# Kernel optimization log

Hardware: AMD Instinct MI355X
Metric: run time of the kernel (lower is better)

Reference implementation:

```python
import jax, jax.numpy as jnp
import numpy as np

B, S, I, H, C = 256, 128, 512, 1024, 10
VOCAB = S  # nn.Embedding(seq_length, input_dim)


def _lstm_dir(embeds_tbi, W, b):
    """Run an LSTM over time. embeds_tbi: [S,B,I]; W: [4H, I+H] stacked (g,i,f,o); b: [4H]."""
    h0 = jnp.zeros((B, H), jnp.float32)
    c0 = jnp.zeros((B, H), jnp.float32)

    def step(carry, x_t):
        c, h = carry
        xh = jnp.concatenate([x_t, h], axis=1)          # [B, I+H]
        z = xh @ W.T + b                                 # [B, 4H]
        g, i, f, o = jnp.split(z, 4, axis=1)
        g = jnp.tanh(g)
        i = jax.nn.sigmoid(i)
        f = jax.nn.sigmoid(f)
        o = jax.nn.sigmoid(o)
        new_c = g * i + c * f
        new_h = jnp.tanh(new_c) * o
        return (new_c, new_h), None

    (c_T, h_T), _ = jax.lax.scan(step, (c0, h0), embeds_tbi)
    return h_T


def setup_inputs() -> dict:
    key = jax.random.key(0)
    ks = jax.random.split(key, 8)
    x = jax.random.randint(ks[0], (B, S), 0, VOCAB)
    embed = jax.random.normal(ks[1], (VOCAB, I), jnp.float32) * 0.5
    scale = 1.0 / np.sqrt(I + H)
    fwd_W = jax.random.normal(ks[2], (4 * H, I + H), jnp.float32) * scale  # stacked g,i,f,o
    fwd_b = jax.random.normal(ks[3], (4 * H,), jnp.float32) * 0.02
    bwd_W = jax.random.normal(ks[4], (4 * H, I + H), jnp.float32) * scale
    bwd_b = jax.random.normal(ks[5], (4 * H,), jnp.float32) * 0.02
    p_w = jax.random.normal(ks[6], (C, 2 * H), jnp.float32) * (1.0 / np.sqrt(2 * H))
    p_b = jax.random.normal(ks[7], (C,), jnp.float32) * 0.02
    return {"x": x, "embed": embed, "fwd_W": fwd_W, "fwd_b": fwd_b,
            "bwd_W": bwd_W, "bwd_b": bwd_b, "p_w": p_w, "p_b": p_b}


def reference(x, embed, fwd_W, fwd_b, bwd_W, bwd_b, p_w, p_b):
    embeds = embed[x]                       # [B,S,I]
    emb_t = jnp.transpose(embeds, (1, 0, 2))  # [S,B,I]
    h_fwd = _lstm_dir(emb_t, fwd_W, fwd_b)
    h_bwd = _lstm_dir(emb_t[::-1], bwd_W, bwd_b)
    h_comb = jnp.concatenate([h_fwd, h_bwd], axis=1)  # [B,2H]
    return jax.nn.log_softmax(h_comb @ p_w.T + p_b, axis=1)
```

## Files before the change

kernel.cpp:

```cpp
#include <hip/hip_runtime.h>
#include <hip/hip_bf16.h>
#include <math.h>

#define B 256
#define S 128
#define I_DIM 512
#define H 1024
#define C 10
#define WROW 1536

#define LDS_H 131072

typedef float f32x4 __attribute__((ext_vector_type(4), may_alias));
typedef __bf16 bf16x8 __attribute__((ext_vector_type(8), may_alias));
typedef unsigned int u32x4 __attribute__((ext_vector_type(4), may_alias));
typedef unsigned long long u64;

__device__ __forceinline__ unsigned short f2bf(float f) {
    union { float f; unsigned u; } a; a.f = f;
    return (unsigned short)((a.u + 0x7fffu + ((a.u >> 16) & 1u)) >> 16);
}
__device__ __forceinline__ float sigf(float v) { return 1.0f / (1.0f + __expf(-v)); }
__device__ __forceinline__ float tanh_fast(float v) { return 1.0f - 2.0f / (1.0f + __expf(2.0f * v)); }

__global__ void wf_build(const float* __restrict__ fwd_W,
                         const float* __restrict__ bwd_W,
                         __hip_bfloat16* __restrict__ wF) {
    int gid = blockIdx.x * 256 + threadIdx.x;
    int lane = gid & 63, kk = (gid >> 6) & 31, nsub = (gid >> 11) & 255, d = gid >> 19;
    int n_gl = nsub * 16 + (lane & 15);
    int j = n_gl >> 2, g = n_gl & 3;
    int k = kk * 32 + (lane >> 4) * 8;
    const float* W = d ? bwd_W : fwd_W;
    const float* src = W + (size_t)(g * 1024 + j) * WROW + I_DIM + k;
    ushort4 lo = make_ushort4(f2bf(src[0]), f2bf(src[1]), f2bf(src[2]), f2bf(src[3]));
    ushort4 hi = make_ushort4(f2bf(src[4]), f2bf(src[5]), f2bf(src[6]), f2bf(src[7]));
    ushort4* dst = (ushort4*)(wF + (size_t)gid * 8);
    dst[0] = lo; dst[1] = hi;
}

__global__ void projp_kernel(const float* __restrict__ embed,
                             const float* __restrict__ fwd_W,
                             const float* __restrict__ fwd_b,
                             const float* __restrict__ bwd_W,
                             const float* __restrict__ bwd_b,
                             float* __restrict__ projP) {
    __shared__ float wrows[16][516];
    int d  = blockIdx.x >> 8;
    int nc = blockIdx.x & 255;
    int n0 = nc * 16;
    const float* W    = d ? bwd_W : fwd_W;
    const float* bias = d ? bwd_b : fwd_b;
    int tid = threadIdx.x;
    for (int i = tid; i < 16 * 128; i += 256) {
        int r = i >> 7, kc = i & 127;
        *(f32x4*)&wrows[r][kc * 4] = *(const f32x4*)(W + (size_t)(n0 + r) * WROW + kc * 4);
    }
    __syncthreads();
    const int r = tid & 15, vg = tid >> 4;
    const float* eb = embed + (size_t)(vg * 8) * I_DIM;
    f32x4 acc[8] = {};
    for (int kc = 0; kc < 128; kc++) {
        f32x4 w = *(const f32x4*)&wrows[r][kc * 4];
#pragma unroll
        for (int vi = 0; vi < 8; vi++) {
            f32x4 e = *(const f32x4*)(eb + (size_t)vi * I_DIM + kc * 4);
            acc[vi] += w * e;
        }
    }
    const int n = n0 + r, g = n >> 10, j = n & 1023;
    const float bv = bias[n];
    float* outp = projP + ((size_t)d * 1024 + j) * 128 * 4 + g;
#pragma unroll
    for (int vi = 0; vi < 8; vi++) {
        float s = acc[vi][0] + acc[vi][1] + acc[vi][2] + acc[vi][3] + bv;
        outp[(vg * 8 + vi) * 4] = s;
    }
}

__device__ __forceinline__ void stage8(const __hip_bfloat16* hr, int r0, int cc,
                                       char* smem, int ibase) {
    const void* p0 = (const void*)(hr + (size_t)((ibase + 0) * 4 + r0) * H + cc * 8);
    const void* p1 = (const void*)(hr + (size_t)((ibase + 1) * 4 + r0) * H + cc * 8);
    const void* p2 = (const void*)(hr + (size_t)((ibase + 2) * 4 + r0) * H + cc * 8);
    const void* p3 = (const void*)(hr + (size_t)((ibase + 3) * 4 + r0) * H + cc * 8);
    const void* p4 = (const void*)(hr + (size_t)((ibase + 4) * 4 + r0) * H + cc * 8);
    const void* p5 = (const void*)(hr + (size_t)((ibase + 5) * 4 + r0) * H + cc * 8);
    const void* p6 = (const void*)(hr + (size_t)((ibase + 6) * 4 + r0) * H + cc * 8);
    const void* p7 = (const void*)(hr + (size_t)((ibase + 7) * 4 + r0) * H + cc * 8);
    u32x4 s0, s1, s2, s3, s4, s5, s6, s7;
    asm volatile(
        "global_load_dwordx4 %0, %8, off sc0 sc1\n\t"
        "global_load_dwordx4 %1, %9, off sc0 sc1\n\t"
        "global_load_dwordx4 %2, %10, off sc0 sc1\n\t"
        "global_load_dwordx4 %3, %11, off sc0 sc1\n\t"
        "global_load_dwordx4 %4, %12, off sc0 sc1\n\t"
        "global_load_dwordx4 %5, %13, off sc0 sc1\n\t"
        "global_load_dwordx4 %6, %14, off sc0 sc1\n\t"
        "global_load_dwordx4 %7, %15, off sc0 sc1\n\t"
        "s_waitcnt vmcnt(0)"
        : "=&v"(s0), "=&v"(s1), "=&v"(s2), "=&v"(s3),
          "=&v"(s4), "=&v"(s5), "=&v"(s6), "=&v"(s7)
        : "v"(p0), "v"(p1), "v"(p2), "v"(p3), "v"(p4), "v"(p5), "v"(p6), "v"(p7)
        : "memory");
    int row;
    row = (ibase + 0) * 4 + r0; *(u32x4*)(smem + row * 2048 + ((cc * 16) ^ ((row & 7) << 4))) = s0;
    row = (ibase + 1) * 4 + r0; *(u32x4*)(smem + row * 2048 + ((cc * 16) ^ ((row & 7) << 4))) = s1;
    row = (ibase + 2) * 4 + r0; *(u32x4*)(smem + row * 2048 + ((cc * 16) ^ ((row & 7) << 4))) = s2;
    row = (ibase + 3) * 4 + r0; *(u32x4*)(smem + row * 2048 + ((cc * 16) ^ ((row & 7) << 4))) = s3;
    row = (ibase + 4) * 4 + r0; *(u32x4*)(smem + row * 2048 + ((cc * 16) ^ ((row & 7) << 4))) = s4;
    row = (ibase + 5) * 4 + r0; *(u32x4*)(smem + row * 2048 + ((cc * 16) ^ ((row & 7) << 4))) = s5;
    row = (ibase + 6) * 4 + r0; *(u32x4*)(smem + row * 2048 + ((cc * 16) ^ ((row & 7) << 4))) = s6;
    row = (ibase + 7) * 4 + r0; *(u32x4*)(smem + row * 2048 + ((cc * 16) ^ ((row & 7) << 4))) = s7;
}

__global__ __launch_bounds__(512, 2) void bilstm_persistent(
        const int* __restrict__ x,
        const __hip_bfloat16* __restrict__ wF,
        const float* __restrict__ projP,
        __hip_bfloat16* __restrict__ hbuf,
        unsigned* __restrict__ flags) {
    extern __shared__ char smem[];
    const int bid = blockIdx.x;
    const int xcd = bid & 7;
    const int d = xcd >> 2, jtHi = xcd & 3;
    const int idx = bid >> 3;
    const int jtLo = idx >> 2, bt = idx & 3;
    const int jt = jtHi * 8 + jtLo;
    const int tid = threadIdx.x, wid = tid >> 6, lane = tid & 63;
    const int l15 = lane & 15, l4 = lane >> 4;
    const int b0 = bt * 64;
    const size_t dBH = (size_t)d * B * H;

    const __hip_bfloat16* wp = wF + (size_t)(d * 256 + jt * 8 + wid) * 16384;
    const int j = jt * 32 + wid * 4 + l4;
    const f32x4* pp = (const f32x4*)projP + ((size_t)d * 1024 + j) * 128;
    const int r0 = tid >> 7;
    const int cc = tid & 127;

    int brow[4], bswz[4];
#pragma unroll
    for (int bs = 0; bs < 4; bs++) {
        int row = bs * 16 + l15;
        brow[bs] = row * 2048;
        bswz[bs] = (row & 7) << 4;
    }

    float cst[4] = {0.f, 0.f, 0.f, 0.f};

    for (int t = 0; t < S; t++) {
        if (t > 0) {
            if (tid == 0) {
                const unsigned* p = flags + (size_t)((t - 1) * 8 + d * 4 + bt) * 16;
                while (__hip_atomic_load(p, __ATOMIC_RELAXED, __HIP_MEMORY_SCOPE_AGENT) < 32u)
                    __builtin_amdgcn_s_sleep(4);
            }
            __syncthreads();
        }

        bf16x8 Ap[8];
        if (t > 0) {
#pragma unroll
            for (int p = 0; p < 8; p++)
                Ap[p] = *(const bf16x8*)(wp + p * 512 + lane * 8);
        }
        const int tt = d ? (S - 1 - t) : t;
        int vv[4];
#pragma unroll
        for (int bs = 0; bs < 4; bs++)
            vv[bs] = x[(b0 + bs * 16 + l15) * S + tt];

        if (t > 0) {
            const __hip_bfloat16* hr = hbuf + (size_t)(t & 1) * 2 * B * H + dBH + (size_t)b0 * H;
            stage8(hr, r0, cc, smem, 0);
            stage8(hr, r0, cc, smem, 8);
        }

        f32x4 pj[4];
#pragma unroll
        for (int bs = 0; bs < 4; bs++) pj[bs] = pp[vv[bs]];

        f32x4 acc[4] = {};
        if (t > 0) {
            __syncthreads();
            bf16x8 Bcur[4];
#pragma unroll
            for (int bs = 0; bs < 4; bs++)
                Bcur[bs] = *(const bf16x8*)(smem + brow[bs] + ((l4 * 16) ^ bswz[bs]));
#pragma unroll
            for (int kk = 0; kk < 32; kk++) {
                bf16x8 A = Ap[kk & 7];
                if (kk < 24)
                    Ap[kk & 7] = *(const bf16x8*)(wp + (kk + 8) * 512 + lane * 8);
                bf16x8 B0 = Bcur[0], B1 = Bcur[1], B2 = Bcur[2], B3 = Bcur[3];
                if (kk < 31) {
                    int koff = (kk + 1) * 64 + l4 * 16;
#pragma unroll
                    for (int bs = 0; bs < 4; bs++)
                        Bcur[bs] = *(const bf16x8*)(smem + brow[bs] + (koff ^ bswz[bs]));
                }
                acc[0] = __builtin_amdgcn_mfma_f32_16x16x32_bf16(A, B0, acc[0], 0, 0, 0);
                acc[1] = __builtin_amdgcn_mfma_f32_16x16x32_bf16(A, B1, acc[1], 0, 0, 0);
                acc[2] = __builtin_amdgcn_mfma_f32_16x16x32_bf16(A, B2, acc[2], 0, 0, 0);
                acc[3] = __builtin_amdgcn_mfma_f32_16x16x32_bf16(A, B3, acc[3], 0, 0, 0);
            }
        }

        float hnv[4];
#pragma unroll
        for (int bs = 0; bs < 4; bs++) {
            float zg = acc[bs][0] + pj[bs][0];
            float zi = acc[bs][1] + pj[bs][1];
            float zf = acc[bs][2] + pj[bs][2];
            float zo = acc[bs][3] + pj[bs][3];
            float gg = tanh_fast(zg);
            float ii = sigf(zi);
            float ff = sigf(zf);
            float oo = sigf(zo);
            float cn = gg * ii + cst[bs] * ff;
            cst[bs] = cn;
            hnv[bs] = tanh_fast(cn) * oo;
        }

        unsigned plo = (unsigned)f2bf(hnv[0]) | ((unsigned)f2bf(hnv[1]) << 16);
        unsigned phi = (unsigned)f2bf(hnv[2]) | ((unsigned)f2bf(hnv[3]) << 16);
        unsigned short o4[4];
#pragma unroll
        for (int p = 0; p < 4; p++) {
            int src = p * 16 + l15;
            unsigned vlo = __shfl(plo, src);
            unsigned vhi = __shfl(phi, src);
            unsigned sel = (l4 < 2) ? vlo : vhi;
            o4[p] = (l4 & 1) ? (unsigned short)(sel >> 16) : (unsigned short)(sel & 0xffffu);
        }
        u64 hv = (u64)o4[0] | ((u64)o4[1] << 16) | ((u64)o4[2] << 32) | ((u64)o4[3] << 48);
        void* hw = (void*)(hbuf + (size_t)((t + 1) & 1) * 2 * B * H + dBH
                           + (size_t)(b0 + lane) * H + jt * 32 + wid * 4);
        asm volatile("global_store_dwordx2 %0, %1, off sc0 sc1"
                     :: "v"(hw), "v"(hv) : "memory");

        __syncthreads();
        if (tid == 0)
            __hip_atomic_fetch_add(flags + (size_t)(t * 8 + d * 4 + bt) * 16, 1u,
                                   __ATOMIC_RELAXED, __HIP_MEMORY_SCOPE_AGENT);
    }
}

__global__ void head_kernel(const __hip_bfloat16* __restrict__ hbuf,
                            const float* __restrict__ p_w,
                            const float* __restrict__ p_b,
                            float* __restrict__ out) {
    int b = blockIdx.x;
    int lane = threadIdx.x;
    float part[C];
#pragma unroll
    for (int cc = 0; cc < C; cc++) part[cc] = 0.0f;
    for (int jj = lane; jj < 2 * H; jj += 64) {
        float hv = (jj < H)
            ? __bfloat162float(hbuf[(size_t)b * H + jj])
            : __bfloat162float(hbuf[(size_t)B * H + (size_t)b * H + jj - H]);
#pragma unroll
        for (int cc = 0; cc < C; cc++) part[cc] += hv * p_w[cc * 2 * H + jj];
    }
#pragma unroll
    for (int cc = 0; cc < C; cc++) {
        float v = part[cc];
        for (int off = 32; off; off >>= 1) v += __shfl_down(v, off);
        part[cc] = v;
    }
    if (lane == 0) {
        float lg[C];
        float m = -1e30f;
        for (int cc = 0; cc < C; cc++) {
            lg[cc] = part[cc] + p_b[cc];
            m = fmaxf(m, lg[cc]);
        }
        float s = 0.0f;
        for (int cc = 0; cc < C; cc++) s += expf(lg[cc] - m);
        float lse = logf(s) + m;
        for (int cc = 0; cc < C; cc++) out[b * C + cc] = lg[cc] - lse;
    }
}

extern "C" void kernel_launch(void* const* d_in, const int* in_sizes, int n_in,
                              void* d_out, int out_size, void* d_ws, size_t ws_size,
                              hipStream_t stream) {
    const int*   x     = (const int*)d_in[0];
    const float* embed = (const float*)d_in[1];
    const float* fwd_W = (const float*)d_in[2];
    const float* fwd_b = (const float*)d_in[3];
    const float* bwd_W = (const float*)d_in[4];
    const float* bwd_b = (const float*)d_in[5];
    const float* p_w   = (const float*)d_in[6];
    const float* p_b   = (const float*)d_in[7];
    float* outp = (float*)d_out;

    char* ws = (char*)d_ws;
    __hip_bfloat16* wF = (__hip_bfloat16*)ws;  ws += (size_t)2 * 256 * 16384 * 2;
    float* projP = (float*)ws;                 ws += (size_t)2 * 1024 * 128 * 4 * 4;
    __hip_bfloat16* hbuf = (__hip_bfloat16*)ws; ws += (size_t)2 * 2 * B * H * 2;
    unsigned* flags = (unsigned*)ws;           ws += (size_t)S * 8 * 16 * 4;

    hipMemsetAsync(flags, 0, (size_t)S * 8 * 16 * 4, stream);
    hipLaunchKernelGGL(wf_build, dim3(4096), dim3(256), 0, stream, fwd_W, bwd_W, wF);
    hipLaunchKernelGGL(projp_kernel, dim3(512), dim3(256), 0, stream,
                       embed, fwd_W, fwd_b, bwd_W, bwd_b, projP);

    hipFuncSetAttribute((const void*)bilstm_persistent,
                        hipFuncAttributeMaxDynamicSharedMemorySize, LDS_H);

    void* args[] = {(void*)&x, (void*)&wF, (void*)&projP, (void*)&hbuf, (void*)&flags};
    hipLaunchCooperativeKernel((void*)bilstm_persistent, dim3(256), dim3(512),
                               args, LDS_H, stream);

    hipLaunchKernelGGL(head_kernel, dim3(B), dim3(64), 0, stream,
                       hbuf, p_w, p_b, outp);
}
```

Baseline: 1.546 ms.

## Keep recurrent weights resident in registers with split-K across wave pairs

Result: slower. 2.174 ms (+40.6%).

```diff
diff --git a/kernel.cpp b/kernel.cpp
--- a/kernel.cpp
+++ b/kernel.cpp
@@ -10,6 +10,8 @@
 #define WROW 1536
 
 #define LDS_H 131072
+#define REDOFF 131072
+#define LDS_TOTAL 163840
 
 typedef float f32x4 __attribute__((ext_vector_type(4), may_alias));
 typedef __bf16 bf16x8 __attribute__((ext_vector_type(8), may_alias));
@@ -122,21 +124,21 @@
         unsigned* __restrict__ flags) {
     extern __shared__ char smem[];
     const int bid = blockIdx.x;
-    const int xcd = bid & 7;
-    const int d = xcd >> 2, jtHi = xcd & 3;
-    const int idx = bid >> 3;
-    const int jtLo = idx >> 2, bt = idx & 3;
-    const int jt = jtHi * 8 + jtLo;
+    const int d = bid >> 7, bt = (bid >> 5) & 3, jt = bid & 31;
     const int tid = threadIdx.x, wid = tid >> 6, lane = tid & 63;
+    const int kq = wid & 1, ngrp = wid >> 1;
     const int l15 = lane & 15, l4 = lane >> 4;
     const int b0 = bt * 64;
     const size_t dBH = (size_t)d * B * H;
 
-    const __hip_bfloat16* wp = wF + (size_t)(d * 256 + jt * 8 + wid) * 16384;
-    const int j = jt * 32 + wid * 4 + l4;
-    const f32x4* pp = (const f32x4*)projP + ((size_t)d * 1024 + j) * 128;
-    const int r0 = tid >> 7;
-    const int cc = tid & 127;
+    bf16x8 wfr[2][16];
+#pragma unroll
+    for (int nt = 0; nt < 2; nt++)
+#pragma unroll
+        for (int kk = 0; kk < 16; kk++)
+            wfr[nt][kk] = *(const bf16x8*)(wF +
+                ((size_t)(d * 256 + jt * 8 + ngrp * 2 + nt) * 32 + kq * 16 + kk) * 512
+                + lane * 8);
 
     int brow[4], bswz[4];
 #pragma unroll
@@ -145,8 +147,9 @@
         brow[bs] = row * 2048;
         bswz[bs] = (row & 7) << 4;
     }
-
-    float cst[4] = {0.f, 0.f, 0.f, 0.f};
+    const int r0 = tid >> 7, cc = tid & 127;
+    const int jb = jt * 32 + ngrp * 8;
+    float cst[2][4] = {};
 
     for (int t = 0; t < S; t++) {
         if (t > 0) {
@@ -158,86 +161,100 @@
             __syncthreads();
         }
 
-        bf16x8 Ap[8];
-        if (t > 0) {
-#pragma unroll
-            for (int p = 0; p < 8; p++)
-                Ap[p] = *(const bf16x8*)(wp + p * 512 + lane * 8);
-        }
         const int tt = d ? (S - 1 - t) : t;
         int vv[4];
-#pragma unroll
-        for (int bs = 0; bs < 4; bs++)
-            vv[bs] = x[(b0 + bs * 16 + l15) * S + tt];
+        if (!kq) {
+#pragma unroll
+            for (int bs = 0; bs < 4; bs++)
+                vv[bs] = x[(b0 + bs * 16 + l15) * S + tt];
+        }
 
         if (t > 0) {
             const __hip_bfloat16* hr = hbuf + (size_t)(t & 1) * 2 * B * H + dBH + (size_t)b0 * H;
             stage8(hr, r0, cc, smem, 0);
             stage8(hr, r0, cc, smem, 8);
-        }
-
-        f32x4 pj[4];
-#pragma unroll
-        for (int bs = 0; bs < 4; bs++) pj[bs] = pp[vv[bs]];
-
-        f32x4 acc[4] = {};
+            __syncthreads();
+        }
+
+        f32x4 acc[2][4] = {};
         if (t > 0) {
+            const int kob = kq * 1024;
+#pragma unroll
+            for (int kk = 0; kk < 16; kk++) {
+                bf16x8 Bf[4];
+                const int koff = kob + kk * 64 + l4 * 16;
+#pragma unroll
+                for (int bs = 0; bs < 4; bs++)
+                    Bf[bs] = *(const bf16x8*)(smem + brow[bs] + (koff ^ bswz[bs]));
+#pragma unroll
+                for (int nt = 0; nt < 2; nt++)
+#pragma unroll
+                    for (int bs = 0; bs < 4; bs++)
+                        acc[nt][bs] = __builtin_amdgcn_mfma_f32_16x16x32_bf16(
+                            wfr[nt][kk], Bf[bs], acc[nt][bs], 0, 0, 0);
+            }
+            if (kq) {
+#pragma unroll
+                for (int nt = 0; nt < 2; nt++)
+#pragma unroll
+                    for (int bs = 0; bs < 4; bs++)
+                        *(f32x4*)(smem + REDOFF +
+                                  ((ngrp * 8 + nt * 4 + bs) * 64 + lane) * 16) = acc[nt][bs];
+            }
             __syncthreads();
-            bf16x8 Bcur[4];
-#pragma unroll
-            for (int bs = 0; bs < 4; bs++)
-                Bcur[bs] = *(const bf16x8*)(smem + brow[bs] + ((l4 * 16) ^ bswz[bs]));
-#pragma unroll
-            for (int kk = 0; kk < 32; kk++) {
-                bf16x8 A = Ap[kk & 7];
-                if (kk < 24)
-                    Ap[kk & 7] = *(const bf16x8*)(wp + (kk + 8) * 512 + lane * 8);
-                bf16x8 B0 = Bcur[0], B1 = Bcur[1], B2 = Bcur[2], B3 = Bcur[3];
-                if (kk < 31) {
-                    int koff = (kk + 1) * 64 + l4 * 16;
+            if (!kq) {
+#pragma unroll
+                for (int nt = 0; nt < 2; nt++)
 #pragma unroll
                     for (int bs = 0; bs < 4; bs++)
-                        Bcur[bs] = *(const bf16x8*)(smem + brow[bs] + (koff ^ bswz[bs]));
+                        acc[nt][bs] += *(const f32x4*)(smem + REDOFF +
+                                  ((ngrp * 8 + nt * 4 + bs) * 64 + lane) * 16);
+            }
+        }
+
+        if (!kq) {
+            unsigned o8[4];
+#pragma unroll
+            for (int nt = 0; nt < 2; nt++) {
+                const int jj = jb + nt * 4 + l4;
+                const f32x4* pp = (const f32x4*)projP + ((size_t)d * 1024 + jj) * 128;
+                float hnv[4];
+#pragma unroll
+                for (int bs = 0; bs < 4; bs++) {
+                    f32x4 pj = pp[vv[bs]];
+                    float zg = acc[nt][bs][0] + pj[0];
+                    float zi = acc[nt][bs][1] + pj[1];
+                    float zf = acc[nt][bs][2] + pj[2];
+                    float zo = acc[nt][bs][3] + pj[3];
+                    float gg = tanh_fast(zg);
+                    float ii = sigf(zi);
+                    float ff = sigf(zf);
+                    float oo = sigf(zo);
+                    float cn = gg * ii + cst[nt][bs] * ff;
+                    cst[nt][bs] = cn;
+                    hnv[bs] = tanh_fast(cn) * oo;
                 }
-                acc[0] = __builtin_amdgcn_mfma_f32_16x16x32_bf16(A, B0, acc[0], 0, 0, 0);
-                acc[1] = __builtin_amdgcn_mfma_f32_16x16x32_bf16(A, B1, acc[1], 0, 0, 0);
-                acc[2] = __builtin_amdgcn_mfma_f32_16x16x32_bf16(A, B2, acc[2], 0, 0, 0);
-                acc[3] = __builtin_amdgcn_mfma_f32_16x16x32_bf16(A, B3, acc[3], 0, 0, 0);
-            }
-        }
-
-        float hnv[4];
-#pragma unroll
-        for (int bs = 0; bs < 4; bs++) {
-            float zg = acc[bs][0] + pj[bs][0];
-            float zi = acc[bs][1] + pj[bs][1];
-            float zf = acc[bs][2] + pj[bs][2];
-            float zo = acc[bs][3] + pj[bs][3];
-            float gg = tanh_fast(zg);
-            float ii = sigf(zi);
-            float ff = sigf(zf);
-            float oo = sigf(zo);
-            float cn = gg * ii + cst[bs] * ff;
-            cst[bs] = cn;
-            hnv[bs] = tanh_fast(cn) * oo;
-        }
-
-        unsigned plo = (unsigned)f2bf(hnv[0]) | ((unsigned)f2bf(hnv[1]) << 16);
-        unsigned phi = (unsigned)f2bf(hnv[2]) | ((unsigned)f2bf(hnv[3]) << 16);
-        unsigned short o4[4];
-#pragma unroll
-        for (int p = 0; p < 4; p++) {
-            int src = p * 16 + l15;
-            unsigned vlo = __shfl(plo, src);
-            unsigned vhi = __shfl(phi, src);
-            unsigned sel = (l4 < 2) ? vlo : vhi;
-            o4[p] = (l4 & 1) ? (unsigned short)(sel >> 16) : (unsigned short)(sel & 0xffffu);
-        }
-        u64 hv = (u64)o4[0] | ((u64)o4[1] << 16) | ((u64)o4[2] << 32) | ((u64)o4[3] << 48);
-        void* hw = (void*)(hbuf + (size_t)((t + 1) & 1) * 2 * B * H + dBH
-                           + (size_t)(b0 + lane) * H + jt * 32 + wid * 4);
-        asm volatile("global_store_dwordx2 %0, %1, off sc0 sc1"
-                     :: "v"(hw), "v"(hv) : "memory");
+                unsigned plo = (unsigned)f2bf(hnv[0]) | ((unsigned)f2bf(hnv[1]) << 16);
+                unsigned phi = (unsigned)f2bf(hnv[2]) | ((unsigned)f2bf(hnv[3]) << 16);
+                unsigned short o4[4];
+#pragma unroll
+                for (int p = 0; p < 4; p++) {
+                    int src = p * 16 + l15;
+                    unsigned vlo = __shfl(plo, src);
+                    unsigned vhi = __shfl(phi, src);
+                    unsigned sel = (l4 < 2) ? vlo : vhi;
+                    o4[p] = (l4 & 1) ? (unsigned short)(sel >> 16)
+                                     : (unsigned short)(sel & 0xffffu);
+                }
+                o8[nt * 2 + 0] = (unsigned)o4[0] | ((unsigned)o4[1] << 16);
+                o8[nt * 2 + 1] = (unsigned)o4[2] | ((unsigned)o4[3] << 16);
+            }
+            u32x4 hv = {o8[0], o8[1], o8[2], o8[3]};
+            void* hw = (void*)(hbuf + (size_t)((t + 1) & 1) * 2 * B * H + dBH
+                               + (size_t)(b0 + lane) * H + jt * 32 + ngrp * 8);
+            asm volatile("global_store_dwordx4 %0, %1, off sc0 sc1"
+                         :: "v"(hw), "v"(hv) : "memory");
+        }
 
         __syncthreads();
         if (tid == 0)
@@ -307,11 +324,11 @@
                        embed, fwd_W, fwd_b, bwd_W, bwd_b, projP);
 
     hipFuncSetAttribute((const void*)bilstm_persistent,
-                        hipFuncAttributeMaxDynamicSharedMemorySize, LDS_H);
+                        hipFuncAttributeMaxDynamicSharedMemorySize, LDS_TOTAL);
 
     void* args[] = {(void*)&x, (void*)&wF, (void*)&projP, (void*)&hbuf, (void*)&flags};
     hipLaunchCooperativeKernel((void*)bilstm_persistent, dim3(256), dim3(512),
-                               args, LDS_H, stream);
+                               args, LDS_TOTAL, stream);
 
     hipLaunchKernelGGL(head_kernel, dim3(B), dim3(64), 0, stream,
                        hbuf, p_w, p_b, outp);
```
